# Optimization experiments

Measured on AMD Instinct MI355X. Metric: run time of the kernel, lower is better.

## Reference

```python
import jax, jax.numpy as jnp
from jax import lax
import numpy as np

T, B, P, A = 1000, 8192, 1024, 4
ER_DECAY = 1.0 - 1e-3  # per-trial exploration-rate decay


def setup_inputs() -> dict:
    key = jax.random.key(0)
    k1, k2, k3, k4 = jax.random.split(key, 4)
    params = jax.random.normal(k1, (13, P), dtype=jnp.float32) * 0.5
    choices = jax.random.randint(k2, (T, B), 0, A, dtype=jnp.int32)
    rewards = (jax.random.uniform(k3, (T, B)) < 0.5).astype(jnp.float32)
    pids = jax.random.randint(k4, (B,), 0, P, dtype=jnp.int32)
    return {"params": params, "rewards": rewards, "choices": choices, "pids": pids}


def _transform_params(params, pids):
    p = jnp.clip(params, -5.0, 5.0)
    sp, sg = jax.nn.softplus, jax.nn.sigmoid
    beta_r = jnp.clip(sp(p[0]), 0.01, 20.0)[pids]
    lapse = jnp.clip(sg(p[1]), 0.01, 0.99)[pids]
    prior = jnp.clip(sp(p[2]), 0.01, 0.99)[pids]
    alpha_er = jnp.clip(sg(p[3]), 0.01, 0.99)[pids]
    decay = jnp.clip(sg(p[4]), 0.01, 0.99)[pids]
    ab1 = p[5][pids]
    ab2 = p[6][pids]
    perv = sp(p[7])[pids]
    sw = p[8][pids]
    gam = sp(p[10])[pids]
    temp = jnp.clip(sp(p[11]) + 1e-6, 1e-6, 100.0)[pids]
    beta_p = sp(p[12])[pids]
    return beta_r, lapse, prior, alpha_er, decay, ab1, ab2, perv, sw, gam, temp, beta_p


def _forward(params, rewards, choices, pids):
    (beta_r, lapse, prior, alpha_er, decay, ab1, ab2,
     perv, sw, gam, temp, beta_p) = _transform_params(params, pids)
    nB = rewards.shape[1]

    q0 = prior[:, None] * jnp.ones((nB, A), dtype=rewards.dtype)
    carry0 = (q0,
              -jnp.ones((nB,), jnp.int32),          # old_choice
              jnp.zeros((nB,), rewards.dtype),       # trials since last switch
              alpha_er,                              # exploration rate
              jnp.zeros((nB, A), rewards.dtype))     # cumulative choice counts

    def step(carry, xs):
        q, old_choice, tsls, er, cum = carry
        choice, reward = xs                       # (B,), (B,)
        oh = jax.nn.one_hot(choice, A, dtype=q.dtype)        # (B, A)
        target = reward - gam * (1.0 - reward)                # loss-averse target
        q = q * (1.0 - oh) + oh * target[:, None]             # q[choice] = target
        same = choice == old_choice
        tsls = jnp.where(same, tsls + 1.0, 0.0)
        er = er * ER_DECAY
        cum = cum + oh
        # exploration smoothing toward mean, then decay
        q = (1.0 - er)[:, None] * q + er[:, None] * q.mean(-1, keepdims=True)
        q = q * decay[:, None]
        sm_in = beta_r[:, None] * q / temp[:, None] + beta_p[:, None] * jnp.log1p(cum)
        probs = (1.0 - lapse)[:, None] * jax.nn.softmax(sm_in, axis=-1) + lapse[:, None] / A
        cl = jnp.log(probs)
        samef = same.astype(q.dtype)[:, None]
        cl = (cl
              + samef * perv[:, None] * oh
              + (1.0 - samef) * sw[:, None] * oh
              + ab1[:, None] * jax.nn.one_hot(old_choice, A, dtype=q.dtype)  # old_choice=-1 -> zeros
              + ab2[:, None] * jax.nn.one_hot((choice + 2) % A, A, dtype=q.dtype)
              + oh * jnp.log(tsls + 1.0)[:, None])
        return (q, choice, tsls, er, cum), cl

    _, logits = lax.scan(step, carry0, (choices, rewards))
    return logits  # (T, B, A)


def reference(params, rewards, choices, pids):
    return _forward(params, rewards, choices, pids)
```

## Files before the change

kernel.cpp:

```cpp
#include <hip/hip_runtime.h>
#include <stdint.h>

#define T_TRIALS 1000
#define B_SIZE   8192
#define P_SIZE   1024
#define CHUNK    32
#define KCH      32
#define NM       31
#define BPB      16
#define BP       17
#define ER_DECAY 0.999f
#define LN_ER_DECAY (-1.0005003335835335e-3f)
#define LOG2E_F 1.4426950408889634f
#define LN2_F   0.69314718055994531f

typedef float f32x4_t __attribute__((ext_vector_type(4)));

__device__ __forceinline__ float sp_(float x){ return __logf(1.0f + __expf(x)); }
__device__ __forceinline__ float sg_(float x){ return 1.0f / (1.0f + __expf(-x)); }
__device__ __forceinline__ float clampf(float x, float lo, float hi){ return fminf(fmaxf(x, lo), hi); }

__global__ __launch_bounds__(512)
void castro_fused2(const float* __restrict__ params,
                   const float* __restrict__ rewards,
                   const int*   __restrict__ choices,
                   const int*   __restrict__ pids,
                   float4*      __restrict__ out4)
{
    __shared__ float4 smap0[NM][BP];
    __shared__ float4 smap1[NM][BP];
    __shared__ float4 smap2[NM][BP];
    __shared__ float4 smap3[NM][BP];
    __shared__ float4 smap4[NM][BP];
    __shared__ float2 smeta[NM][BP];
    __shared__ float4 scpA[KCH][BPB];
    __shared__ float4 scpB[KCH][BPB];

    const int tid = threadIdx.x;
    const int k   = tid >> 4;
    const int bi  = tid & 15;
    const int b   = blockIdx.x * BPB + bi;
    const int t0  = k * CHUNK;
    const int pid = pids[b];

    float p[13];
    #pragma unroll
    for (int kk = 0; kk < 13; ++kk)
        p[kk] = clampf(params[kk * P_SIZE + pid], -5.0f, 5.0f);

    const float beta_r   = clampf(sp_(p[0]), 0.01f, 20.0f);
    const float lapse    = clampf(sg_(p[1]), 0.01f, 0.99f);
    const float prior    = clampf(sp_(p[2]), 0.01f, 0.99f);
    const float alpha_er = clampf(sg_(p[3]), 0.01f, 0.99f);
    const float decay    = clampf(sg_(p[4]), 0.01f, 0.99f);
    const float ab1      = p[5];
    const float ab2      = p[6];
    const float perv     = sp_(p[7]);
    const float sw       = p[8];
    const float gam      = sp_(p[10]);
    const float temp     = clampf(sp_(p[11]) + 1e-6f, 1e-6f, 100.0f);
    const float beta_p   = sp_(p[12]);

    const float bt2 = (beta_r / temp) * LOG2E_F;
    const float ol  = 1.0f - lapse;
    const float la4 = 0.25f * lapse;
    const float gp1 = 1.0f + gam;

    const int*   cp = choices + (size_t)t0 * B_SIZE + b;
    const float* rp = rewards + (size_t)t0 * B_SIZE + b;

    uint32_t wr[4] = {0u, 0u, 0u, 0u};

    if (k < NM) {
        float er = alpha_er * __expf((float)t0 * LN_ER_DECAY);

        float m00=1.f,m01=0.f,m02=0.f,m03=0.f;
        float m10=0.f,m11=1.f,m12=0.f,m13=0.f;
        float m20=0.f,m21=0.f,m22=1.f,m23=0.f;
        float m30=0.f,m31=0.f,m32=0.f,m33=1.f;
        float b0=0.f,b1=0.f,b2=0.f,b3=0.f;
        int   c0=0,c1=0,c2=0,c3=0;
        int   run=0, last=-1;

        #pragma unroll
        for (int g = 0; g < 4; ++g) {
            int cc[8]; float rr[8];
            #pragma unroll
            for (int i = 0; i < 8; ++i) {
                cc[i] = cp[(size_t)(g*8 + i) * B_SIZE];
                rr[i] = rp[(size_t)(g*8 + i) * B_SIZE];
            }
            uint32_t gw = 0;
            #pragma unroll
            for (int i = 0; i < 8; ++i) {
                const int   c = cc[i];
                const float r = rr[i];
                gw |= ((uint32_t)c | (r > 0.5f ? 4u : 0u)) << (4*i);

                er *= ER_DECAY;
                const float target = fmaf(r, gp1, -gam);
                const bool e0=(c==0), e1=(c==1), e2=(c==2), e3=(c==3);

                m00=e0?0.f:m00; m01=e0?0.f:m01; m02=e0?0.f:m02; m03=e0?0.f:m03; b0=e0?target:b0;
                m10=e1?0.f:m10; m11=e1?0.f:m11; m12=e1?0.f:m12; m13=e1?0.f:m13; b1=e1?target:b1;
                m20=e2?0.f:m20; m21=e2?0.f:m21; m22=e2?0.f:m22; m23=e2?0.f:m23; b2=e2?target:b2;
                m30=e3?0.f:m30; m31=e3?0.f:m31; m32=e3?0.f:m32; m33=e3?0.f:m33; b3=e3?target:b3;

                const float s0=(m00+m10)+(m20+m30);
                const float s1=(m01+m11)+(m21+m31);
                const float s2=(m02+m12)+(m22+m32);
                const float s3=(m03+m13)+(m23+m33);
                const float sb=(b0+b1)+(b2+b3);
                const float a  = decay * (1.0f - er);
                const float e4 = decay * er * 0.25f;

                m00=fmaf(e4,s0,a*m00); m01=fmaf(e4,s1,a*m01); m02=fmaf(e4,s2,a*m02); m03=fmaf(e4,s3,a*m03);
                m10=fmaf(e4,s0,a*m10); m11=fmaf(e4,s1,a*m11); m12=fmaf(e4,s2,a*m12); m13=fmaf(e4,s3,a*m13);
                m20=fmaf(e4,s0,a*m20); m21=fmaf(e4,s1,a*m21); m22=fmaf(e4,s2,a*m22); m23=fmaf(e4,s3,a*m23);
                m30=fmaf(e4,s0,a*m30); m31=fmaf(e4,s1,a*m31); m32=fmaf(e4,s2,a*m32); m33=fmaf(e4,s3,a*m33);
                b0=fmaf(e4,sb,a*b0); b1=fmaf(e4,sb,a*b1); b2=fmaf(e4,sb,a*b2); b3=fmaf(e4,sb,a*b3);

                c0 += e0; c1 += e1; c2 += e2; c3 += e3;
                run = (c == last) ? run + 1 : 1;
                last = c;
            }
            wr[g] = gw;
        }

        smap0[k][bi] = make_float4(m00,m01,m02,m03);
        smap1[k][bi] = make_float4(m10,m11,m12,m13);
        smap2[k][bi] = make_float4(m20,m21,m22,m23);
        smap3[k][bi] = make_float4(m30,m31,m32,m33);
        smap4[k][bi] = make_float4(b0,b1,b2,b3);
        const int meta0 = c0 | (c1<<8) | (c2<<16) | (c3<<24);
        const int meta1 = last | (run<<8);
        smeta[k][bi] = make_float2(__int_as_float(meta0), __int_as_float(meta1));
    } else {
        uint32_t gw = 0;
        #pragma unroll
        for (int i = 0; i < 8; ++i) {
            const int   c = cp[(size_t)i * B_SIZE];
            const float r = rp[(size_t)i * B_SIZE];
            gw |= ((uint32_t)c | (r > 0.5f ? 4u : 0u)) << (4*i);
        }
        wr[0] = gw;
    }

    __syncthreads();

    if (tid < BPB) {
        float q0=prior, q1=prior, q2=prior, q3=prior;
        int n0=0,n1=0,n2=0,n3=0;
        int g_run=0, g_last=-1;

        for (int k2 = 0; k2 < KCH; ++k2) {
            const float er_k = alpha_er * __expf((float)(k2*CHUNK) * LN_ER_DECAY);
            const int   tsls = (g_run > 0) ? (g_run - 1) : 0;
            scpA[k2][tid] = make_float4(q0,q1,q2,q3);
            scpB[k2][tid] = make_float4(er_k,
                                        __int_as_float(n0 | (n1<<16)),
                                        __int_as_float(n2 | (n3<<16)),
                                        __int_as_float((tsls & 0xFFFF) | (g_last<<16)));
            if (k2 < NM) {
                const float4 r0 = smap0[k2][tid];
                const float4 r1 = smap1[k2][tid];
                const float4 r2 = smap2[k2][tid];
                const float4 r3 = smap3[k2][tid];
                const float4 r4 = smap4[k2][tid];
                const float2 r5 = smeta[k2][tid];
                const float nq0 = fmaf(r0.w,q3, fmaf(r0.z,q2, fmaf(r0.y,q1, fmaf(r0.x,q0, r4.x))));
                const float nq1 = fmaf(r1.w,q3, fmaf(r1.z,q2, fmaf(r1.y,q1, fmaf(r1.x,q0, r4.y))));
                const float nq2 = fmaf(r2.w,q3, fmaf(r2.z,q2, fmaf(r2.y,q1, fmaf(r2.x,q0, r4.z))));
                const float nq3 = fmaf(r3.w,q3, fmaf(r3.z,q2, fmaf(r3.y,q1, fmaf(r3.x,q0, r4.w))));
                q0=nq0; q1=nq1; q2=nq2; q3=nq3;

                const int meta0 = __float_as_int(r5.x);
                const int meta1 = __float_as_int(r5.y);
                n0 += ( meta0        & 255);
                n1 += ((meta0 >> 8 ) & 255);
                n2 += ((meta0 >> 16) & 255);
                n3 += ((meta0 >> 24) & 255);
                const int last = meta1 & 255;
                const int rn   = meta1 >> 8;
                g_run  = (rn == CHUNK && last == g_last) ? g_run + CHUNK : rn;
                g_last = last;
            }
        }
    }
    __syncthreads();

    {
        const float4 sA = scpA[k][bi];
        const float4 sB = scpB[k][bi];
        float q0=sA.x, q1=sA.y, q2=sA.z, q3=sA.w;
        float er = sB.x;
        const int u1 = __float_as_int(sB.y);
        const int u2 = __float_as_int(sB.z);
        const int u3 = __float_as_int(sB.w);
        float f0 = (float)(u1 & 0xFFFF), f1 = (float)(u1 >> 16);
        float f2 = (float)(u2 & 0xFFFF), f3 = (float)(u2 >> 16);
        float ft = (float)(u3 & 0xFFFF);
        int   old_c = u3 >> 16;

        float bpl0 = beta_p * __log2f(1.0f + f0);
        float bpl1 = beta_p * __log2f(1.0f + f1);
        float bpl2 = beta_p * __log2f(1.0f + f2);
        float bpl3 = beta_p * __log2f(1.0f + f3);

        float4* op = out4 + (size_t)t0 * B_SIZE + b;
        const int ngroups = (k == KCH-1) ? 1 : 4;

        #pragma unroll
        for (int g = 0; g < 4; ++g) {
            if (g < ngroups) {
                uint32_t word = wr[g];
                #pragma unroll
                for (int i = 0; i < 8; ++i) {
                    const int   code = (int)(word & 0xFu); word >>= 4;
                    const int   c    = code & 3;
                    const float r    = (float)((code >> 2) & 1);

                    const float target = fmaf(r, gp1, -gam);
                    const bool e0=(c==0), e1=(c==1), e2=(c==2), e3=(c==3);
                    q0 = e0 ? target : q0;
                    q1 = e1 ? target : q1;
                    q2 = e2 ? target : q2;
                    q3 = e3 ? target : q3;

                    const bool same = (c == old_c);
                    ft = same ? ft + 1.0f : 0.0f;
                    er *= ER_DECAY;

                    const float fsel = e0 ? f0 : (e1 ? f1 : (e2 ? f2 : f3));
                    const float bplc = beta_p * __log2f(fsel + 2.0f);
                    f0 += e0 ? 1.0f : 0.0f;
                    f1 += e1 ? 1.0f : 0.0f;
                    f2 += e2 ? 1.0f : 0.0f;
                    f3 += e3 ? 1.0f : 0.0f;
                    bpl0 = e0 ? bplc : bpl0;
                    bpl1 = e1 ? bplc : bpl1;
                    bpl2 = e2 ? bplc : bpl2;
                    bpl3 = e3 ? bplc : bpl3;

                    const float qm = 0.25f * ((q0+q1)+(q2+q3));
                    q0 = decay * fmaf(er, qm - q0, q0);
                    q1 = decay * fmaf(er, qm - q1, q1);
                    q2 = decay * fmaf(er, qm - q2, q2);
                    q3 = decay * fmaf(er, qm - q3, q3);

                    const float s0 = fmaf(bt2, q0, bpl0);
                    const float s1 = fmaf(bt2, q1, bpl1);
                    const float s2 = fmaf(bt2, q2, bpl2);
                    const float s3 = fmaf(bt2, q3, bpl3);

                    const float m  = fmaxf(fmaxf(s0, s1), fmaxf(s2, s3));
                    const float x0 = exp2f(s0 - m);
                    const float x1 = exp2f(s1 - m);
                    const float x2 = exp2f(s2 - m);
                    const float x3 = exp2f(s3 - m);
                    const float inv = __builtin_amdgcn_rcpf((x0+x1)+(x2+x3));
                    const float sc  = ol * inv;

                    const float L0 = __log2f(fmaf(sc, x0, la4));
                    const float L1 = __log2f(fmaf(sc, x1, la4));
                    const float L2 = __log2f(fmaf(sc, x2, la4));
                    const float L3 = __log2f(fmaf(sc, x3, la4));

                    const float bonus = fmaf(LN2_F, __log2f(ft + 1.0f), same ? perv : sw);

                    float a0 = (e0 ? bonus : 0.0f) + ((old_c == 0) ? ab1 : 0.0f);
                    float a1 = (e1 ? bonus : 0.0f) + ((old_c == 1) ? ab1 : 0.0f);
                    float a2 = (e2 ? bonus : 0.0f) + ((old_c == 2) ? ab1 : 0.0f);
                    float a3 = (e3 ? bonus : 0.0f) + ((old_c == 3) ? ab1 : 0.0f);
                    const int c2 = (c + 2) & 3;
                    a0 += (c2 == 0) ? ab2 : 0.0f;
                    a1 += (c2 == 1) ? ab2 : 0.0f;
                    a2 += (c2 == 2) ? ab2 : 0.0f;
                    a3 += (c2 == 3) ? ab2 : 0.0f;

                    f32x4_t v = { fmaf(LN2_F, L0, a0), fmaf(LN2_F, L1, a1),
                                  fmaf(LN2_F, L2, a2), fmaf(LN2_F, L3, a3) };
                    __builtin_nontemporal_store(v,
                        reinterpret_cast<f32x4_t*>(op + (size_t)(g*8 + i) * B_SIZE));
                    old_c = c;
                }
            }
        }
    }
}

extern "C" void kernel_launch(void* const* d_in, const int* in_sizes, int n_in,
                              void* d_out, int out_size, void* d_ws, size_t ws_size,
                              hipStream_t stream)
{
    const float* params  = (const float*)d_in[0];
    const float* rewards = (const float*)d_in[1];
    const int*   choices = (const int*)  d_in[2];
    const int*   pids    = (const int*)  d_in[3];

    hipLaunchKernelGGL(castro_fused2, dim3(B_SIZE/BPB), dim3(512), 0, stream,
                       params, rewards, choices, pids, (float4*)d_out);
}
```

Before: 63.96 us.

## Halve chunk length to 16 trials and reuse shared buffers for checkpoints

Cuts the per-thread chunk from 32 to 16 trials and the batch rows per block from 16 to 8, giving 63 chunks per row and doubling the grid. Checkpoints are now written in place into the consumed affine-map shared slots, replacing the separate scpA/scpB arrays, and most parameter transforms run on 8 threads and are shared through shared memory to save registers. The aim is shorter serial chains per thread and more blocks in flight. The cost is a sequential scan that is twice as long (62 steps) on a single thread per row, plus more total map composition work.

```diff
diff --git a/kernel.cpp b/kernel.cpp
--- a/kernel.cpp
+++ b/kernel.cpp
@@ -4,13 +4,13 @@
 #define T_TRIALS 1000
 #define B_SIZE   8192
 #define P_SIZE   1024
-#define CHUNK    32
-#define KCH      32
-#define NM       31
-#define BPB      16
-#define BP       17
+#define CHUNK    16
+#define KSLOT    64
+#define KREAL    63
+#define NM       62
+#define BPB      8
 #define ER_DECAY 0.999f
-#define LN_ER_DECAY (-1.0005003335835335e-3f)
+#define ER_L2D   (-1.4434228e-3f)
 #define LOG2E_F 1.4426950408889634f
 #define LN2_F   0.69314718055994531f
 
@@ -21,58 +21,68 @@
 __device__ __forceinline__ float clampf(float x, float lo, float hi){ return fminf(fmaxf(x, lo), hi); }
 
 __global__ __launch_bounds__(512)
-void castro_fused2(const float* __restrict__ params,
+void castro_fused3(const float* __restrict__ params,
                    const float* __restrict__ rewards,
                    const int*   __restrict__ choices,
                    const int*   __restrict__ pids,
                    float4*      __restrict__ out4)
 {
-    __shared__ float4 smap0[NM][BP];
-    __shared__ float4 smap1[NM][BP];
-    __shared__ float4 smap2[NM][BP];
-    __shared__ float4 smap3[NM][BP];
-    __shared__ float4 smap4[NM][BP];
-    __shared__ float2 smeta[NM][BP];
-    __shared__ float4 scpA[KCH][BPB];
-    __shared__ float4 scpB[KCH][BPB];
+    __shared__ float4 smap0[NM][BPB];
+    __shared__ float4 smap1[NM][BPB];
+    __shared__ float4 smap2[NM][BPB];
+    __shared__ float4 smap3[NM][BPB];
+    __shared__ float4 smap4[NM][BPB];
+    __shared__ float2 smeta[NM][BPB];
+    __shared__ float  pshare[BPB][10];
 
     const int tid = threadIdx.x;
-    const int k   = tid >> 4;
-    const int bi  = tid & 15;
+    const int k   = tid >> 3;
+    const int bi  = tid & 7;
     const int b   = blockIdx.x * BPB + bi;
     const int t0  = k * CHUNK;
     const int pid = pids[b];
 
-    float p[13];
-    #pragma unroll
-    for (int kk = 0; kk < 13; ++kk)
-        p[kk] = clampf(params[kk * P_SIZE + pid], -5.0f, 5.0f);
-
-    const float beta_r   = clampf(sp_(p[0]), 0.01f, 20.0f);
-    const float lapse    = clampf(sg_(p[1]), 0.01f, 0.99f);
-    const float prior    = clampf(sp_(p[2]), 0.01f, 0.99f);
-    const float alpha_er = clampf(sg_(p[3]), 0.01f, 0.99f);
-    const float decay    = clampf(sg_(p[4]), 0.01f, 0.99f);
-    const float ab1      = p[5];
-    const float ab2      = p[6];
-    const float perv     = sp_(p[7]);
-    const float sw       = p[8];
-    const float gam      = sp_(p[10]);
-    const float temp     = clampf(sp_(p[11]) + 1e-6f, 1e-6f, 100.0f);
-    const float beta_p   = sp_(p[12]);
-
-    const float bt2 = (beta_r / temp) * LOG2E_F;
-    const float ol  = 1.0f - lapse;
-    const float la4 = 0.25f * lapse;
-    const float gp1 = 1.0f + gam;
+    const float p3  = clampf(params[ 3 * P_SIZE + pid], -5.0f, 5.0f);
+    const float p4  = clampf(params[ 4 * P_SIZE + pid], -5.0f, 5.0f);
+    const float p10 = clampf(params[10 * P_SIZE + pid], -5.0f, 5.0f);
+    const float alpha_er = clampf(sg_(p3), 0.01f, 0.99f);
+    const float decay    = clampf(sg_(p4), 0.01f, 0.99f);
+    const float gam      = sp_(p10);
+    const float gp1      = 1.0f + gam;
+
+    if (tid < BPB) {
+        const float q0_ = clampf(params[ 0 * P_SIZE + pid], -5.0f, 5.0f);
+        const float q1_ = clampf(params[ 1 * P_SIZE + pid], -5.0f, 5.0f);
+        const float q2_ = clampf(params[ 2 * P_SIZE + pid], -5.0f, 5.0f);
+        const float q5_ = clampf(params[ 5 * P_SIZE + pid], -5.0f, 5.0f);
+        const float q6_ = clampf(params[ 6 * P_SIZE + pid], -5.0f, 5.0f);
+        const float q7_ = clampf(params[ 7 * P_SIZE + pid], -5.0f, 5.0f);
+        const float q8_ = clampf(params[ 8 * P_SIZE + pid], -5.0f, 5.0f);
+        const float q11 = clampf(params[11 * P_SIZE + pid], -5.0f, 5.0f);
+        const float q12 = clampf(params[12 * P_SIZE + pid], -5.0f, 5.0f);
+        const float beta_r = clampf(sp_(q0_), 0.01f, 20.0f);
+        const float lapse  = clampf(sg_(q1_), 0.01f, 0.99f);
+        const float prior  = clampf(sp_(q2_), 0.01f, 0.99f);
+        const float temp   = clampf(sp_(q11) + 1e-6f, 1e-6f, 100.0f);
+        pshare[tid][0] = (beta_r / temp) * LOG2E_F;
+        pshare[tid][1] = 1.0f - lapse;
+        pshare[tid][2] = 0.25f * lapse;
+        pshare[tid][3] = prior;
+        pshare[tid][4] = sp_(q7_);
+        pshare[tid][5] = q8_;
+        pshare[tid][6] = q5_;
+        pshare[tid][7] = q6_;
+        pshare[tid][8] = sp_(q12);
+        pshare[tid][9] = 0.0f;
+    }
 
     const int*   cp = choices + (size_t)t0 * B_SIZE + b;
     const float* rp = rewards + (size_t)t0 * B_SIZE + b;
 
-    uint32_t wr[4] = {0u, 0u, 0u, 0u};
+    uint32_t wr[2] = {0u, 0u};
 
     if (k < NM) {
-        float er = alpha_er * __expf((float)t0 * LN_ER_DECAY);
+        float er = alpha_er * exp2f((float)t0 * ER_L2D);
 
         float m00=1.f,m01=0.f,m02=0.f,m03=0.f;
         float m10=0.f,m11=1.f,m12=0.f,m13=0.f;
@@ -83,7 +93,7 @@
         int   run=0, last=-1;
 
         #pragma unroll
-        for (int g = 0; g < 4; ++g) {
+        for (int g = 0; g < 2; ++g) {
             int cc[8]; float rr[8];
             #pragma unroll
             for (int i = 0; i < 8; ++i) {
@@ -135,7 +145,7 @@
         const int meta0 = c0 | (c1<<8) | (c2<<16) | (c3<<24);
         const int meta1 = last | (run<<8);
         smeta[k][bi] = make_float2(__int_as_float(meta0), __int_as_float(meta1));
-    } else {
+    } else if (k == NM) {
         uint32_t gw = 0;
         #pragma unroll
         for (int i = 0; i < 8; ++i) {
@@ -149,18 +159,20 @@
     __syncthreads();
 
     if (tid < BPB) {
+        const float prior = pshare[tid][3];
         float q0=prior, q1=prior, q2=prior, q3=prior;
         int n0=0,n1=0,n2=0,n3=0;
         int g_run=0, g_last=-1;
 
-        for (int k2 = 0; k2 < KCH; ++k2) {
-            const float er_k = alpha_er * __expf((float)(k2*CHUNK) * LN_ER_DECAY);
-            const int   tsls = (g_run > 0) ? (g_run - 1) : 0;
-            scpA[k2][tid] = make_float4(q0,q1,q2,q3);
-            scpB[k2][tid] = make_float4(er_k,
-                                        __int_as_float(n0 | (n1<<16)),
-                                        __int_as_float(n2 | (n3<<16)),
-                                        __int_as_float((tsls & 0xFFFF) | (g_last<<16)));
+        for (int k2 = 0; k2 < KREAL; ++k2) {
+            if (k2 > 0) {
+                const int tsls = (g_run > 0) ? (g_run - 1) : 0;
+                smap0[k2-1][tid] = make_float4(q0,q1,q2,q3);
+                smap1[k2-1][tid] = make_float4(0.0f,
+                                               __int_as_float(n0 | (n1<<16)),
+                                               __int_as_float(n2 | (n3<<16)),
+                                               __int_as_float((tsls & 0xFFFF) | (g_last<<16)));
+            }
             if (k2 < NM) {
                 const float4 r0 = smap0[k2][tid];
                 const float4 r1 = smap1[k2][tid];
@@ -189,18 +201,35 @@
     }
     __syncthreads();
 
-    {
-        const float4 sA = scpA[k][bi];
-        const float4 sB = scpB[k][bi];
-        float q0=sA.x, q1=sA.y, q2=sA.z, q3=sA.w;
-        float er = sB.x;
-        const int u1 = __float_as_int(sB.y);
-        const int u2 = __float_as_int(sB.z);
-        const int u3 = __float_as_int(sB.w);
-        float f0 = (float)(u1 & 0xFFFF), f1 = (float)(u1 >> 16);
-        float f2 = (float)(u2 & 0xFFFF), f3 = (float)(u2 >> 16);
-        float ft = (float)(u3 & 0xFFFF);
-        int   old_c = u3 >> 16;
+    if (k < KREAL) {
+        const float bt2    = pshare[bi][0];
+        const float ol     = pshare[bi][1];
+        const float la4    = pshare[bi][2];
+        const float prior  = pshare[bi][3];
+        const float perv   = pshare[bi][4];
+        const float sw     = pshare[bi][5];
+        const float ab1    = pshare[bi][6];
+        const float ab2    = pshare[bi][7];
+        const float beta_p = pshare[bi][8];
+
+        float q0,q1,q2,q3, ft;
+        float f0,f1,f2,f3;
+        int   old_c;
+        if (k == 0) {
+            q0=q1=q2=q3=prior; f0=f1=f2=f3=0.f; ft=0.f; old_c=-1;
+        } else {
+            const float4 sA = smap0[k-1][bi];
+            const float4 sB = smap1[k-1][bi];
+            q0=sA.x; q1=sA.y; q2=sA.z; q3=sA.w;
+            const int u1 = __float_as_int(sB.y);
+            const int u2 = __float_as_int(sB.z);
+            const int u3 = __float_as_int(sB.w);
+            f0 = (float)(u1 & 0xFFFF); f1 = (float)(u1 >> 16);
+            f2 = (float)(u2 & 0xFFFF); f3 = (float)(u2 >> 16);
+            ft = (float)(u3 & 0xFFFF);
+            old_c = u3 >> 16;
+        }
+        float er = alpha_er * exp2f((float)t0 * ER_L2D);
 
         float bpl0 = beta_p * __log2f(1.0f + f0);
         float bpl1 = beta_p * __log2f(1.0f + f1);
@@ -208,10 +237,10 @@
         float bpl3 = beta_p * __log2f(1.0f + f3);
 
         float4* op = out4 + (size_t)t0 * B_SIZE + b;
-        const int ngroups = (k == KCH-1) ? 1 : 4;
+        const int ngroups = (k == KREAL-1) ? 1 : 2;
 
         #pragma unroll
-        for (int g = 0; g < 4; ++g) {
+        for (int g = 0; g < 2; ++g) {
             if (g < ngroups) {
                 uint32_t word = wr[g];
                 #pragma unroll
@@ -298,6 +327,6 @@
     const int*   choices = (const int*)  d_in[2];
     const int*   pids    = (const int*)  d_in[3];
 
-    hipLaunchKernelGGL(castro_fused2, dim3(B_SIZE/BPB), dim3(512), 0, stream,
+    hipLaunchKernelGGL(castro_fused3, dim3(B_SIZE/BPB), dim3(512), 0, stream,
                        params, rewards, choices, pids, (float4*)d_out);
 }
```

Result: slower. 84.87 us (+32.7%).
